# Optimization experiments

Hardware: AMD Instinct MI355X
Metric: run time of the kernel (lower is better)

The kernel has to match this reference:

```python
import jax, jax.numpy as jnp
import numpy as np

B, T, H, W, C = 2, 8, 60, 60, 256
HEADS = 8
HD = C // HEADS
WH, WW = 5, 6
SH, SW = 2, 3
N = WH * WW            # 30 tokens per window
NW = (H // WH) * (W // WW)  # 120 windows
HID = 4 * C
SCALE = HD ** -0.5


def _rel_pos_index():
    # standard Swin 2D relative position index, shape (N, N)
    coords = np.stack(np.meshgrid(np.arange(WH), np.arange(WW), indexing='ij')).reshape(2, -1)
    rel = (coords[:, :, None] - coords[:, None, :]).transpose(1, 2, 0).astype(np.int64)
    rel[..., 0] += WH - 1
    rel[..., 1] += WW - 1
    rel[..., 0] *= 2 * WW - 1
    return jnp.asarray(rel.sum(-1))


def _attn_mask():
    # shifted-window attention mask, shape (NW, N, N), values in {0, -100}
    img = np.zeros((H, W))
    cnt = 0
    for hs in (slice(0, -WH), slice(-WH, -SH), slice(-SH, None)):
        for ws in (slice(0, -WW), slice(-WW, -SW), slice(-SW, None)):
            img[hs, ws] = cnt
            cnt += 1
    mw = img.reshape(H // WH, WH, W // WW, WW).transpose(0, 2, 1, 3).reshape(NW, N)
    diff = mw[:, None, :] - mw[:, :, None]
    return jnp.asarray(np.where(diff != 0, -100.0, 0.0).astype(np.float32))


REL_INDEX = _rel_pos_index()
ATTN_MASK = _attn_mask()


def _ln(x, g, b):
    m = x.mean(-1, keepdims=True)
    v = ((x - m) ** 2).mean(-1, keepdims=True)
    return (x - m) / jnp.sqrt(v + 1e-5) * g + b


def setup_inputs() -> dict:
    key = jax.random.key(0)
    ks = jax.random.split(key, 8)
    w_scale = 0.02
    return {
        'x': jax.random.normal(ks[0], (B, T, H, W, C), jnp.float32),
        'contrast_embed': jax.random.normal(ks[1], (B, T, C), jnp.float32),
        'gamma1': jnp.ones((C,), jnp.float32),
        'beta1': jnp.zeros((C,), jnp.float32),
        'Wq': jax.random.normal(ks[2], (C, C), jnp.float32) * w_scale,
        'bq': jnp.zeros((C,), jnp.float32),
        'Wk': jax.random.normal(ks[3], (C, C), jnp.float32) * w_scale,
        'bk': jnp.zeros((C,), jnp.float32),
        'Wv': jax.random.normal(ks[4], (C, C), jnp.float32) * w_scale,
        'bv': jnp.zeros((C,), jnp.float32),
        'rel_bias': jax.random.normal(ks[5], ((2 * WH - 1) * (2 * WW - 1), HEADS), jnp.float32) * w_scale,
        'Wo': jax.random.normal(ks[6], (C, C), jnp.float32) * w_scale,
        'bo': jnp.zeros((C,), jnp.float32),
        'gamma2': jnp.ones((C,), jnp.float32),
        'beta2': jnp.zeros((C,), jnp.float32),
        'W1': jax.random.normal(ks[7], (C, HID), jnp.float32) * w_scale,
        'b1': jnp.zeros((HID,), jnp.float32),
        'W2': jax.random.normal(jax.random.fold_in(key, 99), (HID, C), jnp.float32) * w_scale,
        'b2': jnp.zeros((C,), jnp.float32),
    }


def reference(x, contrast_embed, gamma1, beta1, Wq, bq, Wk, bk, Wv, bv, rel_bias,
              Wo, bo, gamma2, beta2, W1, b1, W2, b2):
    shortcut = x
    xn = _ln(x, gamma1, beta1)
    # cyclic shift (SW-MSA)
    xs = jnp.roll(xn, (-SH, -SW), axis=(2, 3))
    # window partition: (B,T,H,W,C) -> (B*NW, T, N, C)
    w = xs.reshape(B, T, H // WH, WH, W // WW, WW, C)
    w = w.transpose(0, 2, 4, 1, 3, 5, 6).reshape(B * NW, T, N, C)
    # per-contrast positional embedding, broadcast over windows and spatial positions
    pos = jnp.broadcast_to(contrast_embed[:, None, :, None, :], (B, NW, T, 1, C)).reshape(B * NW, T, 1, C)
    wqk = w + pos
    q = (wqk @ Wq + bq).reshape(B * NW, T, N, HEADS, HD)
    k = (wqk @ Wk + bk).reshape(B * NW, T, N, HEADS, HD)
    v = (w @ Wv + bv).reshape(B * NW, T, N, HEADS, HD)
    scores = jnp.einsum('btnhd,btmhd->bthnm', q, k) * SCALE
    bias = rel_bias[REL_INDEX].transpose(2, 0, 1)  # (HEADS, N, N)
    scores = scores + bias
    scores = scores.reshape(B, NW, T, HEADS, N, N) + ATTN_MASK[None, :, None, None]
    attn = jax.nn.softmax(scores, axis=-1).reshape(B * NW, T, HEADS, N, N)
    out = jnp.einsum('bthnm,btmhd->btnhd', attn, v).reshape(B * NW, T, N, C)
    out = out @ Wo + bo
    # window reverse: (B*NW, T, N, C) -> (B, T, H, W, C)
    out = out.reshape(B, H // WH, W // WW, T, WH, WW, C)
    out = out.transpose(0, 3, 1, 4, 2, 5, 6).reshape(B, T, H, W, C)
    out = jnp.roll(out, (SH, SW), axis=(2, 3))
    x1 = shortcut + out
    h = jax.nn.gelu(_ln(x1, gamma2, beta2) @ W1 + b1, approximate=False) @ W2 + b2
    return x1 + h
```

## Files before the change

### kernel.cpp

```cpp
#include <hip/hip_runtime.h>

#define DI __device__ __forceinline__

constexpr int SH_=2, SW_=3;
constexpr int ROWS_=57600;
constexpr float SCALE_=0.17677669529663687f;

typedef unsigned short u16x8 __attribute__((ext_vector_type(8)));
typedef short bf16x8 __attribute__((ext_vector_type(8)));
typedef float f32x4 __attribute__((ext_vector_type(4)));
typedef float f32x16 __attribute__((ext_vector_type(16)));

DI float bf2f(unsigned short u){ return __uint_as_float(((unsigned int)u)<<16); }
DI unsigned short f2bf(float f){
  unsigned int u = __float_as_uint(f);
  u += 0x7fffu + ((u>>16)&1u);
  return (unsigned short)(u>>16);
}
DI float ldf(const void* p, size_t i, int f){
  return f ? ((const float*)p)[i] : bf2f(((const unsigned short*)p)[i]);
}
DI float4 ldf4(const void* p, size_t i, int f){
  if (f) return *((const float4*)((const float*)p + i));
  ushort4 u = *((const ushort4*)((const unsigned short*)p + i));
  return make_float4(bf2f(u.x),bf2f(u.y),bf2f(u.z),bf2f(u.w));
}

DI void gload16(const void* g, void* l){
  __builtin_amdgcn_global_load_lds((const __attribute__((address_space(1))) unsigned int*)g,
                                   (__attribute__((address_space(3))) unsigned int*)l, 16, 0, 0);
}

DI void xcd_remap(int wg, int nb, int nn, int& mt, int& nt){
  const int q = nb>>3, r = nb&7;
  const int x = wg & 7, i = wg >> 3;
  const int base = (x<r) ? x*(q+1) : r*(q+1) + (x-r)*q;
  const int work = base + i;
  mt = work / nn; nt = work - mt*nn;
}

#define WAITV(n) asm volatile("s_waitcnt vmcnt(" #n ")" ::: "memory")

__global__ void k_detect(const unsigned short* __restrict__ xu, int* __restrict__ flag){
  unsigned short u = xu[threadIdx.x*2];
  int insane = ((u>>7)&0xFF) > 0xC0;
  unsigned long long m = __ballot(insane);
  if (threadIdx.x==0) *flag = m ? 1 : 0;
}

__global__ __launch_bounds__(256) void k_prepw(
    const void* __restrict__ Wq, const void* __restrict__ Wk,
    const void* __restrict__ Wv, const void* __restrict__ Wo,
    const void* __restrict__ W1, const void* __restrict__ W2,
    unsigned short* __restrict__ wt, const int* __restrict__ flagp)
{
  const int f = *flagp;
  const void* src; int kb, total; size_t off;
  switch(blockIdx.y){
    case 0: src=Wq; kb=8;  total=65536;  off=0;      break;
    case 1: src=Wk; kb=8;  total=65536;  off=65536;  break;
    case 2: src=Wv; kb=8;  total=65536;  off=131072; break;
    case 3: src=Wo; kb=8;  total=65536;  off=196608; break;
    case 4: src=W1; kb=8;  total=262144; off=262144; break;
    default:src=W2; kb=10; total=262144; off=524288; break;
  }
  const int i = blockIdx.x*256 + threadIdx.x;
  if (i >= total) return;
  const int K = 1<<kb, N = total>>kb;
  const int n = i>>kb, k = i&(K-1);
  wt[off + (size_t)n*K + k] = f2bf(ldf(src, (size_t)k*N + n, f));
}

__global__ __launch_bounds__(256) void k_posqk(const void* __restrict__ ce,
    const unsigned short* __restrict__ wtq, const unsigned short* __restrict__ wtk,
    const void* __restrict__ bq, const void* __restrict__ bk,
    float* __restrict__ posq, float* __restrict__ posk, const int* __restrict__ flagp)
{
  const int f = *flagp;
  const int bt = blockIdx.x, mat = blockIdx.y, co = threadIdx.x;
  __shared__ float ces[256];
  ces[co] = ldf(ce, bt*256+co, f);
  __syncthreads();
  const unsigned short* wr = (mat ? wtk : wtq) + (size_t)co*256;
  float s = ldf(mat ? bk : bq, co, f);
  #pragma unroll
  for (int k0=0;k0<256;k0+=8){
    u16x8 wv = *(const u16x8*)(wr + k0);
    #pragma unroll
    for (int j=0;j<8;++j) s += ces[k0+j]*bf2f(wv[j]);
  }
  (mat ? posk : posq)[bt*256+co] = s;
}

__global__ __launch_bounds__(256) void k_ln1(const void* __restrict__ x,
    const void* __restrict__ g, const void* __restrict__ be,
    unsigned short* __restrict__ xw, unsigned char* __restrict__ rowbt,
    int* __restrict__ srowtab, const int* __restrict__ flagp)
{
  const int f = *flagp;
  const int lane = threadIdx.x & 63;
  const int wv   = threadIdx.x >> 6;
  const int rs   = blockIdx.x*4 + wv;
  float4 u = ldf4(x, (size_t)rs*256 + lane*4, f);
  float s = u.x+u.y+u.z+u.w;
  #pragma unroll
  for (int o=32;o;o>>=1) s += __shfl_xor(s,o,64);
  const float mean = s*(1.f/256.f);
  float d0=u.x-mean, d1=u.y-mean, d2=u.z-mean, d3=u.w-mean;
  float qv = d0*d0+d1*d1+d2*d2+d3*d3;
  #pragma unroll
  for (int o=32;o;o>>=1) qv += __shfl_xor(qv,o,64);
  const float rstd = rsqrtf(qv*(1.f/256.f)+1e-5f);
  float4 gu = ldf4(g, lane*4, f);
  float4 bu = ldf4(be, lane*4, f);
  ushort4 o;
  o.x = f2bf(d0*rstd*gu.x+bu.x);
  o.y = f2bf(d1*rstd*gu.y+bu.y);
  o.z = f2bf(d2*rstd*gu.z+bu.z);
  o.w = f2bf(d3*rstd*gu.w+bu.w);
  const int c = rs % 60, r = (rs/60)%60, t = (rs/3600)&7, b = rs/28800;
  int r2 = r - SH_; if (r2<0) r2+=60;
  int c2 = c - SW_; if (c2<0) c2+=60;
  const int a=r2/5, ii=r2%5, bb=c2/6, jj=c2%6;
  const int rw = ((b*120 + a*10+bb)*8 + t)*30 + ii*6+jj;
  *reinterpret_cast<ushort4*>(xw + (size_t)rw*256 + lane*4) = o;
  if (lane==0){
    rowbt[rw] = (unsigned char)(b*8+t);
    srowtab[rw] = rs;
  }
}

__global__ __launch_bounds__(256) void k_ln2(const unsigned short* __restrict__ x1b,
    const void* __restrict__ g, const void* __restrict__ be,
    unsigned short* __restrict__ xn2, const int* __restrict__ flagp)
{
  const int f = *flagp;
  const int lane = threadIdx.x & 63;
  const int wv   = threadIdx.x >> 6;
  const int rs   = blockIdx.x*4 + wv;
  float4 v = ldf4(x1b, (size_t)rs*256 + lane*4, 0);
  float s = v.x+v.y+v.z+v.w;
  #pragma unroll
  for (int o=32;o;o>>=1) s += __shfl_xor(s,o,64);
  const float mean = s*(1.f/256.f);
  float d0=v.x-mean, d1=v.y-mean, d2=v.z-mean, d3=v.w-mean;
  float qv = d0*d0+d1*d1+d2*d2+d3*d3;
  #pragma unroll
  for (int o=32;o;o>>=1) qv += __shfl_xor(qv,o,64);
  const float rstd = rsqrtf(qv*(1.f/256.f)+1e-5f);
  float4 gu = ldf4(g, lane*4, f);
  float4 bu = ldf4(be, lane*4, f);
  ushort4 o;
  o.x = f2bf(d0*rstd*gu.x+bu.x);
  o.y = f2bf(d1*rstd*gu.y+bu.y);
  o.z = f2bf(d2*rstd*gu.z+bu.z);
  o.w = f2bf(d3*rstd*gu.w+bu.w);
  *reinterpret_cast<ushort4*>(xn2 + (size_t)rs*256 + lane*4) = o;
}

template<int K>
DI void mfma_core128(const unsigned short* __restrict__ A, const unsigned short* __restrict__ WT,
                     const int m0, const int n0, f32x4 acc[4][2], unsigned short* lds)
{
  constexpr int STEPS = K/32;
  const int tid = threadIdx.x, lane = tid&63, wave = tid>>6;
  const int wm = (wave>>2)*64, wn = (wave&3)*32;
  const int fr = lane&15;
  const int kqs = ((lane>>4) ^ ((fr>>1)&3))*8;
  #pragma unroll
  for (int i=0;i<4;++i)
    #pragma unroll
    for (int j=0;j<2;++j) acc[i][j] = (f32x4){0.f,0.f,0.f,0.f};
  const int isB = wave>>2;
  const int c0 = (wave&3)*128 + lane;
  const int c1 = c0 + 64;
  const int r0=c0>>2, p0=((c0&3)^((r0>>1)&3));
  const int r1=c1>>2, p1=((c1&3)^((r1>>1)&3));
  const unsigned short* gb = isB ? (WT + (size_t)n0*K) : (A + (size_t)m0*K);
  const unsigned short* g0 = gb + (size_t)r0*K + p0*8;
  const unsigned short* g1 = gb + (size_t)r1*K + p1*8;
  const int ldso = isB*4096 + (wave&3)*1024;
  #define STAGE_(d,k0) do{ \
    unsigned short* bse = lds + (d)*8192 + ldso; \
    gload16(g0+(k0), bse); \
    gload16(g1+(k0), bse+512); }while(0)
  STAGE_(0,0);
  STAGE_(1,32);
  int cur = 0;
  for (int t=0; t<STEPS; ++t){
    if (t+2 < STEPS){
      int nb = cur+2; if (nb>=3) nb-=3;
      STAGE_(nb, (t+2)*32);
      WAITV(4);
    } else if (t+2 == STEPS){
      WAITV(2);
    } else {
      WAITV(0);
    }
    __builtin_amdgcn_s_barrier();
    const unsigned short* At = lds + cur*8192;
    const unsigned short* Bt = At + 4096;
    bf16x8 af[4], bfv[2];
    #pragma unroll
    for (int mi=0;mi<4;++mi) af[mi]  = *(const bf16x8*)(At + (wm+mi*16+fr)*32 + kqs);
    #pragma unroll
    for (int ni=0;ni<2;++ni) bfv[ni] = *(const bf16x8*)(Bt + (wn+ni*16+fr)*32 + kqs);
    __builtin_amdgcn_s_setprio(1);
    #pragma unroll
    for (int mi=0;mi<4;++mi){
      acc[mi][0] = __builtin_amdgcn_mfma_f32_16x16x32_bf16(af[mi], bfv[0], acc[mi][0], 0,0,0);
      acc[mi][1] = __builtin_amdgcn_mfma_f32_16x16x32_bf16(af[mi], bfv[1], acc[mi][1], 0,0,0);
    }
    __builtin_amdgcn_s_setprio(0);
    __builtin_amdgcn_s_barrier();
    cur = (cur+1==3)?0:cur+1;
  }
  #undef STAGE_
}

__global__ __launch_bounds__(512,5) void k_gemm_qkv(const unsigned short* __restrict__ Ain,
    const unsigned short* __restrict__ WT, const float* __restrict__ posq,
    const float* __restrict__ posk, const void* __restrict__ bv,
    unsigned short* __restrict__ qb, unsigned short* __restrict__ kb,
    unsigned short* __restrict__ vb2, const unsigned char* __restrict__ rowbt,
    const int* __restrict__ flagp)
{
  __shared__ __align__(16) unsigned short lds[24576];
  f32x4 acc[4][2];
  int mt, nt; xcd_remap(blockIdx.x, 2700, 6, mt, nt);
  const int m0 = mt*128;
  mfma_core128<256>(Ain, WT, m0, nt*128, acc, lds);
  const int f = *flagp;
  const int tid = threadIdx.x, lane = tid&63, wave = tid>>6;
  const int wm = (wave>>2)*64, wn = (wave&3)*32;
  const int fr = lane&15, fq = lane>>4;
  const int seg = nt>>1;
  unsigned short* ob = seg==0? qb : (seg==1? kb : vb2);
  const float* posb = seg==0? posq : posk;
  #pragma unroll
  for (int mi=0;mi<4;++mi){
    #pragma unroll
    for (int r=0;r<4;++r){
      const int row = wm+mi*16+fq*4+r;
      const int bt2 = rowbt[m0+row];
      #pragma unroll
      for (int ni=0;ni<2;++ni){
        const int lcol = wn+ni*16+fr;
        const int colm = (nt&1)*128 + lcol;
        const float bvv = (seg<2) ? posb[bt2*256+colm] : ldf(bv,colm,f);
        lds[row*132+lcol] = f2bf(acc[mi][ni][r] + bvv);
      }
    }
  }
  __syncthreads();
  const int row = tid>>2;
  unsigned short* dst = ob + (size_t)(m0+row)*256 + (nt&1)*128;
  #pragma unroll
  for (int j=0;j<4;++j){
    const int ci = j*4 + (tid&3);
    *(u16x8*)(dst + ci*8) = *(const u16x8*)(lds + row*132 + ci*8);
  }
}

__global__ __launch_bounds__(256) void k_attn(const unsigned short* __restrict__ q,
    const unsigned short* __restrict__ k, const unsigned short* __restrict__ v,
    const void* __restrict__ relb, unsigned short* __restrict__ ao,
    const int* __restrict__ flagp)
{
  __shared__ __align__(16) unsigned short vt[4][32*40];
  __shared__ __align__(16) unsigned short pa[4][32*40];
  const int f = *flagp;
  const int tid = threadIdx.x, lane = tid&63, wave = tid>>6;
  const int task = blockIdx.x*4 + wave;
  const int h = task & 7, bt = task >> 3;
  const int wi = (bt>>3) % 120;
  const int a_ = wi/10, bb_ = wi%10;
  const size_t base = (size_t)bt*7680 + h*32;
  unsigned short* vtw = &vt[wave][0];
  unsigned short* paw = &pa[wave][0];
  if (lane < 60){
    const int m = lane>>1, hf = lane&1;
    const unsigned short* src = v + base + (size_t)m*256 + hf*16;
    u16x8 r0 = *(const u16x8*)(src);
    u16x8 r1 = *(const u16x8*)(src+8);
    #pragma unroll
    for (int j=0;j<8;++j){ vtw[(hf*16+j)*40+m] = r0[j]; vtw[(hf*16+8+j)*40+m] = r1[j]; }
  }
  vtw[(lane>>1)*40 + 30 + (lane&1)] = 0;
  const int n  = lane&31;
  const int hl = lane>>5;
  f32x16 accS = {};
  {
    const unsigned short* ka = k + base + (size_t)n*256 + hl*8;
    const unsigned short* qa = q + base + (size_t)n*256 + hl*8;
    bf16x8 a0 = *(const bf16x8*)(ka);
    bf16x8 b0 = *(const bf16x8*)(qa);
    accS = __builtin_amdgcn_mfma_f32_32x32x16_bf16(a0, b0, accS, 0,0,0);
    bf16x8 a1 = *(const bf16x8*)(ka+16);
    bf16x8 b1 = *(const bf16x8*)(qa+16);
    accS = __builtin_amdgcn_mfma_f32_32x32x16_bf16(a1, b1, accS, 0,0,0);
  }
  const int nc  = (n < 30) ? n : 29;
  const int in_ = nc/6, jn = nc - in_*6;
  const int rn = a_*5+in_, cn = bb_*6+jn;
  const int lnl = (rn<55?0:(rn<58?1:2))*3 + (cn<54?0:(cn<57?1:2));
  #pragma unroll
  for (int r=0;r<16;++r){
    const int m = (r&3) + 8*(r>>2) + 4*hl;
    if (m < 30){
      const int im = m/6, jm = m - im*6;
      const int ridx = (in_-im+4)*11 + (jn-jm+5);
      const float bi = ldf(relb, ridx*8+h, f);
      const int rm = a_*5+im, cm = bb_*6+jm;
      const int lml = (rm<55?0:(rm<58?1:2))*3 + (cm<54?0:(cm<57?1:2));
      accS[r] = accS[r]*SCALE_ + bi + (lnl==lml ? 0.f : -100.f);
    } else accS[r] = -1e30f;
  }
  float mx = accS[0];
  #pragma unroll
  for (int r=1;r<16;++r) mx = fmaxf(mx, accS[r]);
  mx = fmaxf(mx, __shfl_xor(mx, 32, 64));
  float sum = 0.f;
  #pragma unroll
  for (int r=0;r<16;++r){ accS[r] = __expf(accS[r]-mx); sum += accS[r]; }
  sum += __shfl_xor(sum, 32, 64);
  const float inv = 1.f/sum;
  #pragma unroll
  for (int r=0;r<16;++r){
    const int m = (r&3)+8*(r>>2)+4*hl;
    paw[n*40 + m] = f2bf(accS[r]);
  }
  f32x16 accO = {};
  #pragma unroll
  for (int ks=0; ks<2; ++ks){
    bf16x8 av  = *(const bf16x8*)(vtw + n*40 + ks*16 + hl*8);
    bf16x8 pv  = *(const bf16x8*)(paw + n*40 + ks*16 + hl*8);
    accO = __builtin_amdgcn_mfma_f32_32x32x16_bf16(av, pv, accO, 0,0,0);
  }
  if (n < 30){
    #pragma unroll
    for (int g4=0; g4<4; ++g4){
      const int d0 = 8*g4 + 4*hl;
      ushort4 o;
      o.x = f2bf(accO[g4*4+0]*inv);
      o.y = f2bf(accO[g4*4+1]*inv);
      o.z = f2bf(accO[g4*4+2]*inv);
      o.w = f2bf(accO[g4*4+3]*inv);
      *(ushort4*)(ao + base + (size_t)n*256 + d0) = o;
    }
  }
}

__global__ __launch_bounds__(512,5) void k_gemm_wo(const unsigned short* __restrict__ Ain,
    const unsigned short* __restrict__ WT, const void* __restrict__ bias,
    const void* __restrict__ xin, unsigned short* __restrict__ x1b,
    const int* __restrict__ srowtab, const int* __restrict__ flagp)
{
  __shared__ __align__(16) unsigned short lds[24576];
  f32x4 acc[4][2];
  int mt, nt; xcd_remap(blockIdx.x, 900, 2, mt, nt);
  const int m0 = mt*128, n0 = nt*128;
  mfma_core128<256>(Ain, WT, m0, n0, acc, lds);
  const int f = *flagp;
  const int tid = threadIdx.x, lane = tid&63, wave = tid>>6;
  const int wm = (wave>>2)*64, wn = (wave&3)*32;
  const int fr = lane&15, fq = lane>>4;
  #pragma unroll
  for (int mi=0;mi<4;++mi){
    #pragma unroll
    for (int ni=0;ni<2;++ni){
      const int lcol = wn+ni*16+fr;
      const float bvv = ldf(bias, n0+lcol, f);
      #pragma unroll
      for (int r=0;r<4;++r){
        const int row = wm+mi*16+fq*4+r;
        lds[row*132+lcol] = f2bf(acc[mi][ni][r] + bvv);
      }
    }
  }
  __syncthreads();
  const int row = tid>>2;
  const size_t srow = (size_t)srowtab[m0+row];
  #pragma unroll
  for (int j=0;j<4;++j){
    const int ci = j*4 + (tid&3);
    const int col = n0 + ci*8;
    u16x8 vv = *(const u16x8*)(lds + row*132 + ci*8);
    float4 xa = ldf4(xin, srow*256+col,   f);
    float4 xbv= ldf4(xin, srow*256+col+4, f);
    u16x8 o;
    o[0]=f2bf(bf2f(vv[0])+xa.x); o[1]=f2bf(bf2f(vv[1])+xa.y);
    o[2]=f2bf(bf2f(vv[2])+xa.z); o[3]=f2bf(bf2f(vv[3])+xa.w);
    o[4]=f2bf(bf2f(vv[4])+xbv.x); o[5]=f2bf(bf2f(vv[5])+xbv.y);
    o[6]=f2bf(bf2f(vv[6])+xbv.z); o[7]=f2bf(bf2f(vv[7])+xbv.w);
    *(u16x8*)(x1b + srow*256 + col) = o;
  }
}

__global__ __launch_bounds__(512,5) void k_mlp1(const unsigned short* __restrict__ Ain,
    const unsigned short* __restrict__ WT, const void* __restrict__ bias,
    unsigned short* __restrict__ hb, const int row0, const int* __restrict__ flagp)
{
  __shared__ __align__(16) unsigned short lds[24576];
  f32x4 acc[4][2];
  int mt, nt; xcd_remap(blockIdx.x, 1800, 8, mt, nt);
  const int m0 = row0 + mt*128, n0 = nt*128;
  mfma_core128<256>(Ain, WT, m0, n0, acc, lds);
  const int f = *flagp;
  const int tid = threadIdx.x, lane = tid&63, wave = tid>>6;
  const int wm = (wave>>2)*64, wn = (wave&3)*32;
  const int fr = lane&15, fq = lane>>4;
  #pragma unroll
  for (int mi=0;mi<4;++mi){
    #pragma unroll
    for (int ni=0;ni<2;++ni){
      const int lcol = wn+ni*16+fr;
      const float bvv = ldf(bias, n0+lcol, f);
      #pragma unroll
      for (int r=0;r<4;++r){
        const int row = wm+mi*16+fq*4+r;
        const float vv = acc[mi][ni][r] + bvv;
        lds[row*132+lcol] = f2bf(0.5f*vv*(1.f+erff(vv*0.70710678118654752f)));
      }
    }
  }
  __syncthreads();
  const int row = tid>>2;
  unsigned short* dst = hb + (size_t)(mt*128+row)*1024 + n0;
  #pragma unroll
  for (int j=0;j<4;++j){
    const int ci = j*4 + (tid&3);
    *(u16x8*)(dst + ci*8) = *(const u16x8*)(lds + row*132 + ci*8);
  }
}

__global__ __launch_bounds__(512,5) void k_mlp2(const unsigned short* __restrict__ hbin,
    const unsigned short* __restrict__ WT, const void* __restrict__ bias,
    const unsigned short* __restrict__ x1b, void* __restrict__ outb,
    const int row0, const int* __restrict__ flagp)
{
  __shared__ __align__(16) unsigned short lds[24576];
  f32x4 acc[4][2];
  int mt, nt; xcd_remap(blockIdx.x, 450, 2, mt, nt);
  const int m0l = mt*128, n0 = nt*128;
  mfma_core128<1024>(hbin, WT, m0l, n0, acc, lds);
  const int f = *flagp;
  const int tid = threadIdx.x, lane = tid&63, wave = tid>>6;
  const int wm = (wave>>2)*64, wn = (wave&3)*32;
  const int fr = lane&15, fq = lane>>4;
  #pragma unroll
  for (int mi=0;mi<4;++mi){
    #pragma unroll
    for (int ni=0;ni<2;++ni){
      const int lcol = wn+ni*16+fr;
      const float bvv = ldf(bias, n0+lcol, f);
      #pragma unroll
      for (int r=0;r<4;++r){
        const int row = wm+mi*16+fq*4+r;
        lds[row*132+lcol] = f2bf(acc[mi][ni][r] + bvv);
      }
    }
  }
  __syncthreads();
  const int row = tid>>2;
  const size_t grow = (size_t)(row0 + m0l + row);
  #pragma unroll
  for (int j=0;j<4;++j){
    const int ci = j*4 + (tid&3);
    const int col = n0 + ci*8;
    u16x8 vv = *(const u16x8*)(lds + row*132 + ci*8);
    u16x8 xv = *(const u16x8*)(x1b + grow*256 + col);
    if (f){
      float4 o0, o1;
      o0.x=bf2f(vv[0])+bf2f(xv[0]); o0.y=bf2f(vv[1])+bf2f(xv[1]);
      o0.z=bf2f(vv[2])+bf2f(xv[2]); o0.w=bf2f(vv[3])+bf2f(xv[3]);
      o1.x=bf2f(vv[4])+bf2f(xv[4]); o1.y=bf2f(vv[5])+bf2f(xv[5]);
      o1.z=bf2f(vv[6])+bf2f(xv[6]); o1.w=bf2f(vv[7])+bf2f(xv[7]);
      *(float4*)((float*)outb + grow*256 + col)     = o0;
      *(float4*)((float*)outb + grow*256 + col + 4) = o1;
    } else {
      u16x8 o;
      #pragma unroll
      for (int e=0;e<8;++e) o[e] = f2bf(bf2f(vv[e])+bf2f(xv[e]));
      *(u16x8*)((unsigned short*)outb + grow*256 + col) = o;
    }
  }
}

extern "C" void kernel_launch(void* const* d_in, const int* in_sizes, int n_in,
                              void* d_out, int out_size, void* d_ws, size_t ws_size,
                              hipStream_t stream)
{
  const void* x   = d_in[0];
  const void* ce  = d_in[1];
  const void* g1  = d_in[2];
  const void* be1 = d_in[3];
  const void* Wq  = d_in[4];
  const void* bq  = d_in[5];
  const void* Wk  = d_in[6];
  const void* bk  = d_in[7];
  const void* Wv  = d_in[8];
  const void* bv  = d_in[9];
  const void* rb  = d_in[10];
  const void* Wo  = d_in[11];
  const void* bo  = d_in[12];
  const void* g2  = d_in[13];
  const void* be2 = d_in[14];
  const void* W1  = d_in[15];
  const void* b1  = d_in[16];
  const void* W2  = d_in[17];
  const void* b2  = d_in[18];

  char* ws = (char*)d_ws;
  const size_t SZ = (size_t)ROWS_*256*2;
  unsigned short* kbuf = (unsigned short*)(ws);
  unsigned short* vbuf = (unsigned short*)(ws + SZ);
  unsigned short* xw   = (unsigned short*)(ws + 2*SZ);
  unsigned short* qbuf = (unsigned short*)(ws + 3*SZ);
  unsigned short* aob  = xw;
  unsigned short* xn2  = kbuf;
  unsigned short* x1b  = qbuf;
  unsigned short* hb   = vbuf;
  float* posq = (float*)(ws + 4*SZ);
  float* posk = posq + 16*256;
  int*   flag = (int*)(ws + 4*SZ + 32768);
  unsigned short* wt = (unsigned short*)(ws + 4*SZ + 65536);
  int*   srowtab = (int*)(ws + 4*SZ + 65536 + 1572864);
  unsigned char* rowbt = (unsigned char*)(ws + 4*SZ + 65536 + 1572864 + 230400);

  unsigned short* wtqkv = wt;
  unsigned short* wtq = wt;
  unsigned short* wtk = wt + 65536;
  unsigned short* wto = wt + 196608;
  unsigned short* wt1 = wt + 262144;
  unsigned short* wt2 = wt + 524288;

  k_detect<<<1,64,0,stream>>>((const unsigned short*)x, flag);
  k_prepw<<<dim3(1024,6),256,0,stream>>>(Wq,Wk,Wv,Wo,W1,W2, wt, flag);
  k_posqk<<<dim3(16,2),256,0,stream>>>(ce, wtq, wtk, bq, bk, posq, posk, flag);
  k_ln1<<<14400,256,0,stream>>>(x, g1, be1, xw, rowbt, srowtab, flag);
  k_gemm_qkv<<<2700,512,0,stream>>>(xw, wtqkv, posq, posk, bv, qbuf, kbuf, vbuf, rowbt, flag);
  k_attn<<<3840,256,0,stream>>>(qbuf, kbuf, vbuf, rb, aob, flag);
  k_gemm_wo<<<900,512,0,stream>>>(aob, wto, bo, x, x1b, srowtab, flag);
  k_ln2<<<14400,256,0,stream>>>(x1b, g2, be2, xn2, flag);
  for (int chk=0; chk<2; ++chk){
    const int row0 = chk*28800;
    k_mlp1<<<1800,512,0,stream>>>(xn2, wt1, b1, hb, row0, flag);
    k_mlp2<<<450,512,0,stream>>>(hb, wt2, b2, x1b, d_out, row0, flag);
  }
}
```

Measured before the change: 272.7 us.

## Widen QKV GEMM tile to 128x256 with double-buffered inline K loop

The QKV projection GEMM now computes a 128x256 output tile per block instead of 128x128, so each block covers a whole Q, K or V segment and the grid is halved. The A tile is loaded once per 256 output columns, which halves A-side global traffic. The shared mfma_core helper is replaced by an inline double-buffered K loop with 4x4 accumulators per wave. The epilogue writes the tile out in two 128-column halves through LDS. This raises register pressure and adds extra syncs in the epilogue, while the launch-bounds hint is raised to 6 blocks.

```diff
diff --git a/kernel.cpp b/kernel.cpp
--- a/kernel.cpp
+++ b/kernel.cpp
@@ -218,7 +218,7 @@
   #undef STAGE_
 }
 
-__global__ __launch_bounds__(512,5) void k_gemm_qkv(const unsigned short* __restrict__ Ain,
+__global__ __launch_bounds__(512,6) void k_gemm_qkv(const unsigned short* __restrict__ Ain,
     const unsigned short* __restrict__ WT, const float* __restrict__ posq,
     const float* __restrict__ posk, const void* __restrict__ bv,
     unsigned short* __restrict__ qb, unsigned short* __restrict__ kb,
@@ -226,39 +226,86 @@
     const int* __restrict__ flagp)
 {
   __shared__ __align__(16) unsigned short lds[24576];
-  f32x4 acc[4][2];
-  int mt, nt; xcd_remap(blockIdx.x, 2700, 6, mt, nt);
-  const int m0 = mt*128;
-  mfma_core128<256>(Ain, WT, m0, nt*128, acc, lds);
-  const int f = *flagp;
+  f32x4 acc[4][4];
+  int mt, nt; xcd_remap(blockIdx.x, 1350, 3, mt, nt);
+  const int m0 = mt*128, n0 = nt*256;
   const int tid = threadIdx.x, lane = tid&63, wave = tid>>6;
-  const int wm = (wave>>2)*64, wn = (wave&3)*32;
+  const int wm = (wave>>2)*64, wn = (wave&3)*64;
   const int fr = lane&15, fq = lane>>4;
-  const int seg = nt>>1;
-  unsigned short* ob = seg==0? qb : (seg==1? kb : vb2);
-  const float* posb = seg==0? posq : posk;
-  #pragma unroll
-  for (int mi=0;mi<4;++mi){
-    #pragma unroll
-    for (int r=0;r<4;++r){
-      const int row = wm+mi*16+fq*4+r;
-      const int bt2 = rowbt[m0+row];
+  const int kqs = ((lane>>4) ^ ((fr>>1)&3))*8;
+  #pragma unroll
+  for (int i=0;i<4;++i)
+    #pragma unroll
+    for (int j=0;j<4;++j) acc[i][j] = (f32x4){0.f,0.f,0.f,0.f};
+  const int rA = tid>>2, pA = (tid&3)^((rA>>1)&3);
+  const int rB2 = 128 + (tid>>2), pB2 = (tid&3)^((rB2>>1)&3);
+  const unsigned short* gA  = Ain + (size_t)(m0+rA)*256 + pA*8;
+  const unsigned short* gB1 = WT + (size_t)(n0+rA)*256 + pA*8;
+  const unsigned short* gB2 = WT + (size_t)(n0+rB2)*256 + pB2*8;
+  const int wb = wave*512;
+  #define STAGEQ_(d,k0) do{ \
+    unsigned short* bse = lds + (d)*12288; \
+    gload16(gA +(k0), bse + wb); \
+    gload16(gB1+(k0), bse + 4096 + wb); \
+    gload16(gB2+(k0), bse + 8192 + wb); }while(0)
+  STAGEQ_(0,0);
+  for (int t=0; t<8; ++t){
+    const int cur = t&1;
+    if (t+1 < 8){
+      STAGEQ_(cur^1, (t+1)*32);
+      WAITV(3);
+    } else {
+      WAITV(0);
+    }
+    __builtin_amdgcn_s_barrier();
+    const unsigned short* At = lds + cur*12288;
+    const unsigned short* Bt = At + 4096;
+    bf16x8 af[4], bfv[4];
+    #pragma unroll
+    for (int mi=0;mi<4;++mi) af[mi]  = *(const bf16x8*)(At + (wm+mi*16+fr)*32 + kqs);
+    #pragma unroll
+    for (int ni=0;ni<4;++ni) bfv[ni] = *(const bf16x8*)(Bt + (wn+ni*16+fr)*32 + kqs);
+    __builtin_amdgcn_s_setprio(1);
+    #pragma unroll
+    for (int mi=0;mi<4;++mi)
       #pragma unroll
-      for (int ni=0;ni<2;++ni){
-        const int lcol = wn+ni*16+fr;
-        const int colm = (nt&1)*128 + lcol;
-        const float bvv = (seg<2) ? posb[bt2*256+colm] : ldf(bv,colm,f);
-        lds[row*132+lcol] = f2bf(acc[mi][ni][r] + bvv);
+      for (int ni=0;ni<4;++ni)
+        acc[mi][ni] = __builtin_amdgcn_mfma_f32_16x16x32_bf16(af[mi], bfv[ni], acc[mi][ni], 0,0,0);
+    __builtin_amdgcn_s_setprio(0);
+    __builtin_amdgcn_s_barrier();
+  }
+  #undef STAGEQ_
+  const int f = *flagp;
+  unsigned short* ob = nt==0? qb : (nt==1? kb : vb2);
+  const float* posb = nt==0? posq : posk;
+  #pragma unroll
+  for (int half=0; half<2; ++half){
+    if (((wave&3)>>1) == half){
+      #pragma unroll
+      for (int mi=0;mi<4;++mi){
+        #pragma unroll
+        for (int r=0;r<4;++r){
+          const int row = wm+mi*16+fq*4+r;
+          const int bt2 = rowbt[m0+row];
+          #pragma unroll
+          for (int ni=0;ni<4;++ni){
+            const int colm = wn + ni*16 + fr;
+            const int lcol = colm & 127;
+            const float bvv = (nt<2) ? posb[bt2*256+colm] : ldf(bv,colm,f);
+            lds[row*132+lcol] = f2bf(acc[mi][ni][r] + bvv);
+          }
+        }
       }
     }
-  }
-  __syncthreads();
-  const int row = tid>>2;
-  unsigned short* dst = ob + (size_t)(m0+row)*256 + (nt&1)*128;
-  #pragma unroll
-  for (int j=0;j<4;++j){
-    const int ci = j*4 + (tid&3);
-    *(u16x8*)(dst + ci*8) = *(const u16x8*)(lds + row*132 + ci*8);
+    __syncthreads();
+    const int row = tid>>2;
+    unsigned short* dst = ob + (size_t)(m0+row)*256 + half*128;
+    #pragma unroll
+    for (int j=0;j<4;++j){
+      const int ci = j*4 + (tid&3);
+      *(u16x8*)(dst + ci*8) = *(const u16x8*)(lds + row*132 + ci*8);
+    }
+    __syncthreads();
   }
 }
 
@@ -539,7 +586,7 @@
   k_prepw<<<dim3(1024,6),256,0,stream>>>(Wq,Wk,Wv,Wo,W1,W2, wt, flag);
   k_posqk<<<dim3(16,2),256,0,stream>>>(ce, wtq, wtk, bq, bk, posq, posk, flag);
   k_ln1<<<14400,256,0,stream>>>(x, g1, be1, xw, rowbt, srowtab, flag);
-  k_gemm_qkv<<<2700,512,0,stream>>>(xw, wtqkv, posq, posk, bv, qbuf, kbuf, vbuf, rowbt, flag);
+  k_gemm_qkv<<<1350,512,0,stream>>>(xw, wtqkv, posq, posk, bv, qbuf, kbuf, vbuf, rowbt, flag);
   k_attn<<<3840,256,0,stream>>>(qbuf, kbuf, vbuf, rb, aob, flag);
   k_gemm_wo<<<900,512,0,stream>>>(aob, wto, bo, x, x1b, srowtab, flag);
   k_ln2<<<14400,256,0,stream>>>(x1b, g2, be2, xn2, flag);
```

New measurement: 491.3 us. +80.1%, slower.
